# Kernel optimization log

Measured on AMD Instinct MI355X. Metric: run time of the kernel, lower is better.

The kernel has to match this reference:

```python
import jax, jax.numpy as jnp
import numpy as np

B, T, IN, RES, OUT = 32, 512, 128, 2048, 64
SPECTRAL_RADIUS = 0.9
LEAKING_RATE = 0.3
INPUT_SCALING = 1.0
WINDOW, OVERLAP = 8, 2


def setup_inputs() -> dict:
    key = jax.random.key(0)
    k1, k2 = jax.random.split(key)
    input_data = jax.random.normal(k1, (B, T, IN), dtype=jnp.float32)
    target_data = jax.random.normal(k2, (B, T, OUT), dtype=jnp.float32)
    rng = np.random.default_rng(0)
    W_res = rng.random((RES, RES), dtype=np.float32) - 0.5
    W_res *= SPECTRAL_RADIUS / np.max(np.abs(np.linalg.eigvals(W_res)))
    W_in = (rng.random((IN, RES), dtype=np.float32) - 0.5) * INPUT_SCALING
    lam_raw = jnp.zeros((), jnp.float32)
    return {"input_data": input_data, "target_data": target_data,
            "W_res": jnp.asarray(W_res.astype(np.float32)),
            "W_in": jnp.asarray(W_in.astype(np.float32)),
            "lam_raw": lam_raw}


def run_reservoir(input_data, W_res, W_in):
    b, t, d = input_data.shape
    out_size = WINDOW - 2 * OVERLAP  # 4
    pad = jnp.zeros((b, OVERLAP, d), input_data.dtype)
    x = jnp.concatenate([pad, input_data, pad], axis=1)  # [B, T+4, D]
    n_win = (t + 2 * OVERLAP - WINDOW) // out_size + 1  # T // 4
    idx = jnp.arange(n_win)[:, None] * out_size + jnp.arange(WINDOW)[None, :]
    xw = x[:, idx, :]  # [B, nW, 8, D] windows (unfold)
    state = jnp.zeros((b, n_win, W_res.shape[0]), input_data.dtype)
    states = []
    for s in range(WINDOW - OVERLAP):  # 6 sequential steps (fixed, small)
        state = (1.0 - LEAKING_RATE) * state + LEAKING_RATE * jnp.sin(
            jnp.einsum('bwr,rq->bwq', state, W_res)
            + jnp.einsum('bwd,dq->bwq', xw[:, :, s, :], W_in))
        states.append(state)
    rs = jnp.stack(states, axis=2)[:, :, OVERLAP:, :]  # keep last 4 per window
    return rs.reshape(b, t, W_res.shape[0])  # [B, T, R]


def ridge_weights(X, Y, reg_coeff):
    b, n, d = X.shape
    Xb = jnp.concatenate([X, jnp.ones((b, n, 1), X.dtype)], axis=-1)  # [B,n,d+1]
    if n >= d + 1:
        A = jnp.einsum('bnd,bne->bde', Xb, Xb) + reg_coeff * jnp.eye(d + 1, dtype=X.dtype)
        Bm = jnp.einsum('bnd,bno->bdo', Xb, Y)
        weights = jnp.linalg.solve(A, Bm)
    else:  # Woodbury: n < d+1
        A = jnp.einsum('bnd,bmd->bnm', Xb, Xb) + reg_coeff * jnp.eye(n, dtype=X.dtype)
        weights = jnp.einsum('bnd,bno->bdo', Xb, jnp.linalg.solve(A, Y))
    return weights[:, :-1], weights[:, -1:]


def reference(input_data, target_data, W_res, W_in, lam_raw):
    rs = run_reservoir(input_data, W_res, W_in)  # [B, T, R]
    reg_coeff = jax.nn.softplus(lam_raw)
    w, bias = ridge_weights(rs, target_data, reg_coeff)
    return (w, bias)
```

## Files before the change

### kernel.cpp

```cpp
#include <hip/hip_runtime.h>
#include <cmath>

#define Bb   32
#define Tt   512
#define INd  128
#define RES  2048
#define OUTd 64

#define BM 64
#define BN 64
#define BK 16

typedef unsigned short u16;
typedef __attribute__((ext_vector_type(4))) unsigned short u16x4;
typedef __attribute__((ext_vector_type(8))) unsigned short u16x8;
typedef __attribute__((ext_vector_type(8))) short bf8;
typedef __attribute__((ext_vector_type(4))) float f32x4;

__device__ __forceinline__ void splitf(float a, u16& h, u16& l) {
    unsigned u = __float_as_uint(a);
    unsigned r = (u + 0x7fffu + ((u >> 16) & 1u)) & 0xffff0000u;
    h = (u16)(r >> 16);
    float d = a - __uint_as_float(r);
    l = (u16)(__float_as_uint(d) >> 16);
}
__device__ __forceinline__ float bf2f(u16 h) {
    return __uint_as_float((unsigned)h << 16);
}
__device__ __forceinline__ void split8(const float4& a, const float4& b,
                                       u16x8& h, u16x8& l) {
    u16 hh, ll;
    splitf(a.x, hh, ll); h[0] = hh; l[0] = ll;
    splitf(a.y, hh, ll); h[1] = hh; l[1] = ll;
    splitf(a.z, hh, ll); h[2] = hh; l[2] = ll;
    splitf(a.w, hh, ll); h[3] = hh; l[3] = ll;
    splitf(b.x, hh, ll); h[4] = hh; l[4] = ll;
    splitf(b.y, hh, ll); h[5] = hh; l[5] = ll;
    splitf(b.z, hh, ll); h[6] = hh; l[6] = ll;
    splitf(b.w, hh, ll); h[7] = hh; l[7] = ll;
}

__device__ __forceinline__ void gl_lds16(const u16* g, u16* l) {
    __builtin_amdgcn_global_load_lds(
        (const __attribute__((address_space(1))) unsigned int*)g,
        (__attribute__((address_space(3))) unsigned int*)l,
        16, 0, 0);
}

#define MICRO(SA, SB)                                                           \
  do {                                                                          \
    _Pragma("unroll")                                                           \
    for (int kk = 0; kk < BK; ++kk) {                                           \
      const float4 a4 = *(const float4*)&SA[kk][ty << 2];                       \
      const float4 b4 = *(const float4*)&SB[kk][tx << 2];                       \
      acc[0][0] += a4.x*b4.x; acc[0][1] += a4.x*b4.y;                           \
      acc[0][2] += a4.x*b4.z; acc[0][3] += a4.x*b4.w;                           \
      acc[1][0] += a4.y*b4.x; acc[1][1] += a4.y*b4.y;                           \
      acc[1][2] += a4.y*b4.z; acc[1][3] += a4.y*b4.w;                           \
      acc[2][0] += a4.z*b4.x; acc[2][1] += a4.z*b4.y;                           \
      acc[2][2] += a4.z*b4.z; acc[2][3] += a4.z*b4.w;                           \
      acc[3][0] += a4.w*b4.x; acc[3][1] += a4.w*b4.y;                           \
      acc[3][2] += a4.w*b4.z; acc[3][3] += a4.w*b4.w;                           \
    }                                                                           \
  } while (0)

#define MFMA_TILE(BUF)                                                           \
  do {                                                                           \
    bf8 aH[4], aL[4], bH[4], bL[4];                                              \
    const int qd = (quad ^ ((l15 >> 1) & 3)) << 3;                               \
    _Pragma("unroll")                                                            \
    for (int i = 0; i < 4; ++i) {                                                \
      const int ar = (wm*64 + i*16 + l15)*32 + qd;                               \
      const int br = (wn*64 + i*16 + l15)*32 + qd;                               \
      aH[i] = *(const bf8*)&(BUF)[ar];                                           \
      aL[i] = *(const bf8*)&(BUF)[4096 + ar];                                    \
      bH[i] = *(const bf8*)&(BUF)[8192 + br];                                    \
      bL[i] = *(const bf8*)&(BUF)[12288 + br];                                   \
    }                                                                            \
    _Pragma("unroll")                                                            \
    for (int i = 0; i < 4; ++i)                                                  \
      _Pragma("unroll")                                                          \
      for (int j = 0; j < 4; ++j) {                                              \
        acc[i][j] = __builtin_amdgcn_mfma_f32_16x16x32_bf16(aH[i], bH[j], acc[i][j], 0, 0, 0); \
        acc[i][j] = __builtin_amdgcn_mfma_f32_16x16x32_bf16(aH[i], bL[j], acc[i][j], 0, 0, 0); \
        acc[i][j] = __builtin_amdgcn_mfma_f32_16x16x32_bf16(aL[i], bH[j], acc[i][j], 0, 0, 0); \
      }                                                                          \
  } while (0)

__global__ __launch_bounds__(256)
void tconv_kernel(const float* __restrict__ in, u16* __restrict__ outH,
                  u16* __restrict__ outL, int K, int N)
{
    __shared__ float T[64][65];
    const int n0 = blockIdx.x * 64, k0 = blockIdx.y * 64;
    const int t = threadIdx.x;
    const int r = t >> 2, c0 = (t & 3) * 16;
#pragma unroll
    for (int i = 0; i < 4; ++i) {
        const float4 v = *(const float4*)&in[(size_t)(k0 + r) * N + n0 + c0 + 4*i];
        T[r][c0 + 4*i + 0] = v.x; T[r][c0 + 4*i + 1] = v.y;
        T[r][c0 + 4*i + 2] = v.z; T[r][c0 + 4*i + 3] = v.w;
    }
    __syncthreads();
    const int n = t >> 2, ck = (t & 3) * 16;
    u16x8 h0, h1, l0, l1;
#pragma unroll
    for (int i = 0; i < 8; ++i) { u16 h, l; splitf(T[ck + i][n], h, l); h0[i] = h; l0[i] = l; }
#pragma unroll
    for (int i = 0; i < 8; ++i) { u16 h, l; splitf(T[ck + 8 + i][n], h, l); h1[i] = h; l1[i] = l; }
    const size_t ob = (size_t)(n0 + n) * K + k0 + ck;
    *(u16x8*)&outH[ob] = h0; *(u16x8*)&outH[ob + 8] = h1;
    *(u16x8*)&outL[ob] = l0; *(u16x8*)&outL[ob + 8] = l1;
}

__global__ __launch_bounds__(256)
void step_mfma_kernel(u16* __restrict__ Sh, u16* __restrict__ Sl,
                      const float* __restrict__ X,
                      const u16* __restrict__ WTh, const u16* __restrict__ WTl,
                      const u16* __restrict__ WinTh, const u16* __restrict__ WinTl,
                      int cin, int cout, int s)
{
    __shared__ u16 LB[2 * 16384];
    u16* buf0 = LB;
    u16* buf1 = LB + 16384;
    float* Cf = (float*)LB;

    const int tid = threadIdx.x;
    const int f  = (int)blockIdx.x + ((int)blockIdx.y << 4);
    const int bx = (f & 1) | (((f >> 3) & 7) << 1);
    const int by = ((f >> 1) & 3) | (((f >> 6) & 7) << 2);
    const int q0  = bx * 128;
    const int b   = by;
    const int bofs = b * Tt;
    const int wid = tid >> 6, lane = tid & 63;
    const int wm = wid & 1, wn = wid >> 1;
    const int l15 = lane & 15, quad = lane >> 4;

    f32x4 acc[4][4];
    const f32x4 zz = {0.f, 0.f, 0.f, 0.f};
#pragma unroll
    for (int i = 0; i < 4; ++i)
#pragma unroll
        for (int j = 0; j < 4; ++j) acc[i][j] = zz;

    const int rl    = lane >> 2;
    const int csrc  = (((lane & 3) ^ ((lane >> 3) & 3)) << 3);
    const u16* plane = (wid == 0) ? (const u16*)Sh
                     : (wid == 1) ? (const u16*)Sl
                     : (wid == 2) ? WTh : WTl;

    auto stage = [&](u16* buf, int k0) {
        u16* ldst = buf + wid * 4096;
#pragma unroll
        for (int i = 0; i < 8; ++i) {
            const int r = i * 16 + rl;
            const size_t grow = (wid < 2) ? (size_t)(bofs + 4 * r + cin)
                                          : (size_t)(q0 + r);
            gl_lds16(&plane[grow * RES + k0 + csrc], ldst + i * 512);
        }
    };

    if (s > 0) {
        stage(buf0, 0);
        __syncthreads();
        for (int k0 = 0; k0 < RES; k0 += 32) {
            u16* cur = (k0 & 32) ? buf1 : buf0;
            u16* nxt = (k0 & 32) ? buf0 : buf1;
            if (k0 + 32 < RES) stage(nxt, k0 + 32);
            MFMA_TILE(cur);
            __syncthreads();
        }
    }

    for (int k0 = 0; k0 < INd; k0 += 32) {
        if (tid < 128) {
            const int rrow = tid;
            const int t = 4 * rrow + s - 2;
            u16x8 h0 = {0,0,0,0,0,0,0,0}, h1 = h0, h2 = h0, h3 = h0;
            u16x8 l0 = h0, l1 = h0, l2 = h0, l3 = h0;
            if (t >= 0) {
                const float* xr = X + (size_t)(bofs + t) * INd + k0;
                const float4 f0 = *(const float4*)&xr[0];
                const float4 f1 = *(const float4*)&xr[4];
                const float4 f2 = *(const float4*)&xr[8];
                const float4 f3 = *(const float4*)&xr[12];
                const float4 f4 = *(const float4*)&xr[16];
                const float4 f5 = *(const float4*)&xr[20];
                const float4 f6 = *(const float4*)&xr[24];
                const float4 f7 = *(const float4*)&xr[28];
                split8(f0, f1, h0, l0); split8(f2, f3, h1, l1);
                split8(f4, f5, h2, l2); split8(f6, f7, h3, l3);
            }
            const int sw = (rrow >> 1) & 3;
            u16* dA = buf0 + rrow * 32;
            *(u16x8*)&dA[(0 ^ sw) << 3] = h0;
            *(u16x8*)&dA[(1 ^ sw) << 3] = h1;
            *(u16x8*)&dA[(2 ^ sw) << 3] = h2;
            *(u16x8*)&dA[(3 ^ sw) << 3] = h3;
            u16* dL = buf0 + 4096 + rrow * 32;
            *(u16x8*)&dL[(0 ^ sw) << 3] = l0;
            *(u16x8*)&dL[(1 ^ sw) << 3] = l1;
            *(u16x8*)&dL[(2 ^ sw) << 3] = l2;
            *(u16x8*)&dL[(3 ^ sw) << 3] = l3;
        } else {
            const u16* wpl = (wid == 2) ? WinTh : WinTl;
            u16* ldst = buf0 + wid * 4096;
#pragma unroll
            for (int i = 0; i < 8; ++i) {
                const int r = i * 16 + rl;
                gl_lds16(&wpl[(size_t)(q0 + r) * INd + k0 + csrc], ldst + i * 512);
            }
        }
        __syncthreads();
        MFMA_TILE(buf0);
        __syncthreads();
    }

    for (int h = 0; h < 2; ++h) {
        __syncthreads();
        if (wm == h) {
#pragma unroll
            for (int i = 0; i < 4; ++i)
#pragma unroll
                for (int j = 0; j < 4; ++j)
#pragma unroll
                    for (int rg = 0; rg < 4; ++rg)
                        Cf[(i * 16 + quad * 4 + rg) * 128 + wn * 64 + j * 16 + l15]
                            = acc[i][j][rg];
        }
        __syncthreads();
#pragma unroll
        for (int pass = 0; pass < 4; ++pass) {
            const int r  = (tid >> 4) + pass * 16;
            const int c0 = (tid & 15) * 8;
            const int wrow = h * 64 + r;
            const float4 v0 = *(const float4*)&Cf[r * 128 + c0];
            const float4 v1 = *(const float4*)&Cf[r * 128 + c0 + 4];
            float vv[8] = {v0.x, v0.y, v0.z, v0.w, v1.x, v1.y, v1.z, v1.w};
            u16x8 ph, pl;
            if (s > 0) {
                const size_t prow = (size_t)(bofs + 4 * wrow + cin) * RES + q0 + c0;
                ph = *(const u16x8*)&Sh[prow];
                pl = *(const u16x8*)&Sl[prow];
            }
            u16x8 oh, ol;
#pragma unroll
            for (int e = 0; e < 8; ++e) {
                float prev = (s > 0) ? (bf2f(ph[e]) + bf2f(pl[e])) : 0.f;
                float v = 0.7f * prev + 0.3f * sinf(vv[e]);
                u16 hh, ll; splitf(v, hh, ll);
                oh[e] = hh; ol[e] = ll;
            }
            const size_t orow = (size_t)(bofs + 4 * wrow + cout) * RES + q0 + c0;
            *(u16x8*)&Sh[orow] = oh;
            *(u16x8*)&Sl[orow] = ol;
        }
    }
}

__global__ __launch_bounds__(256)
void gram_mfma_kernel(const u16* __restrict__ Sh, const u16* __restrict__ Sl,
                      float* __restrict__ A, const float* __restrict__ lam)
{
    __shared__ u16 LB[2 * 16384];
    u16* buf0 = LB;
    u16* buf1 = LB + 16384;
    float* Cf = (float*)LB;

    const int tid = threadIdx.x;
    const int bt  = blockIdx.y;
    int ti = 0, rem = (int)blockIdx.x;
    while (rem >= 4 - ti) { rem -= 4 - ti; ++ti; }
    const int tj = ti + rem;
    const int n0 = ti * 128, m0 = tj * 128;
    const int bofs = bt * Tt;

    const int wid = tid >> 6, lane = tid & 63;
    const int wm = wid & 1, wn = wid >> 1;
    const int l15 = lane & 15, quad = lane >> 4;

    f32x4 acc[4][4];
    const f32x4 zz = {0.f, 0.f, 0.f, 0.f};
#pragma unroll
    for (int i = 0; i < 4; ++i)
#pragma unroll
        for (int j = 0; j < 4; ++j) acc[i][j] = zz;

    const int rl    = lane >> 2;
    const int csrc  = (((lane & 3) ^ ((lane >> 3) & 3)) << 3);
    const u16* plane = (wid & 1) ? Sl : Sh;
    const int rbase  = (wid < 2) ? n0 : m0;

    auto stage = [&](u16* buf, int k0) {
        u16* ldst = buf + wid * 4096;
#pragma unroll
        for (int i = 0; i < 8; ++i) {
            const int r = i * 16 + rl;
            gl_lds16(&plane[(size_t)(bofs + rbase + r) * RES + k0 + csrc],
                     ldst + i * 512);
        }
    };

    stage(buf0, 0);
    __syncthreads();
    for (int k0 = 0; k0 < RES; k0 += 32) {
        u16* cur = (k0 & 32) ? buf1 : buf0;
        u16* nxt = (k0 & 32) ? buf0 : buf1;
        if (k0 + 32 < RES) stage(nxt, k0 + 32);
        MFMA_TILE(cur);
        __syncthreads();
    }

    const float reg = log1pf(expf(lam[0]));
    float* Ab = A + (size_t)bt * 512 * 512;
    for (int h = 0; h < 2; ++h) {
        __syncthreads();
        if (wm == h) {
#pragma unroll
            for (int i = 0; i < 4; ++i)
#pragma unroll
                for (int j = 0; j < 4; ++j)
#pragma unroll
                    for (int rg = 0; rg < 4; ++rg)
                        Cf[(i * 16 + quad * 4 + rg) * 132 + wn * 64 + j * 16 + l15]
                            = acc[i][j][rg];
        }
        __syncthreads();
#pragma unroll
        for (int pass = 0; pass < 4; ++pass) {
            const int r  = (tid >> 4) + pass * 16;
            const int c0 = (tid & 15) * 8;
            const int nn = n0 + h * 64 + r;
            float o[8];
#pragma unroll
            for (int e = 0; e < 8; ++e) {
                const int mm = m0 + c0 + e;
                float v = Cf[r * 132 + c0 + e] + 1.0f;
                if (nn == mm) v += reg;
                o[e] = v;
            }
            float* dst = Ab + (size_t)nn * 512 + m0 + c0;
            *(float4*)&dst[0] = make_float4(o[0], o[1], o[2], o[3]);
            *(float4*)&dst[4] = make_float4(o[4], o[5], o[6], o[7]);
        }
#pragma unroll
        for (int pass = 0; pass < 4; ++pass) {
            const int rt  = (tid >> 3) + pass * 32;
            const int c0t = (tid & 7) * 8;
            const int mm  = m0 + rt;
            float o[8];
#pragma unroll
            for (int e = 0; e < 8; ++e) {
                const int nn = n0 + h * 64 + c0t + e;
                float v = Cf[(c0t + e) * 132 + rt] + 1.0f;
                if (nn == mm) v += reg;
                o[e] = v;
            }
            float* dst = Ab + (size_t)mm * 512 + n0 + h * 64 + c0t;
            *(float4*)&dst[0] = make_float4(o[0], o[1], o[2], o[3]);
            *(float4*)&dst[4] = make_float4(o[4], o[5], o[6], o[7]);
        }
    }
}

__global__ __launch_bounds__(256)
void chol_diag_inv_kernel(float* __restrict__ Aall, float* __restrict__ Winv,
                          float* __restrict__ WinvT, int k)
{
    __shared__ float P[64][65];
    __shared__ float W[64][65];
    const int b = blockIdx.x, tid = threadIdx.x;
    float* A = Aall + (size_t)b * 512 * 512;
    const int j0 = 64 * k;
    const int r = tid & 63;
    const int q = tid >> 6;

    {
        const int lr = tid >> 2, lc = (tid & 3) * 16;
#pragma unroll
        for (int i = 0; i < 4; ++i) {
            const float4 v = *(const float4*)(A + (size_t)(j0 + lr) * 512 + j0 + lc + 4*i);
            P[lr][lc + 4*i + 0] = v.x; P[lr][lc + 4*i + 1] = v.y;
            P[lr][lc + 4*i + 2] = v.z; P[lr][lc + 4*i + 3] = v.w;
        }
    }
    __syncthreads();

    for (int j = 0; j < 64; ++j) {
        if (tid < 64) {
            const float d = sqrtf(P[j][j]);
            if (tid == j)      P[j][j]   = d;
            else if (tid > j)  P[tid][j] = P[tid][j] / d;
        }
        __syncthreads();
        const float prj = P[r][j];
        float pm[16];
#pragma unroll
        for (int i = 0; i < 16; ++i) pm[i] = P[q * 16 + i][j];
#pragma unroll
        for (int i = 0; i < 16; ++i) {
            const int m = q * 16 + i;
            if (m > j && m <= r) P[r][m] -= prj * pm[i];
        }
        __syncthreads();
    }

    for (int t = tid; t < 4096; t += 256)
        W[t >> 6][t & 63] = ((t >> 6) == (t & 63)) ? 1.f : 0.f;
    __syncthreads();
    for (int j = 0; j < 64; ++j) {
        if (tid < 64) W[j][tid] = W[j][tid] / P[j][j];
        __syncthreads();
        const float wjc = W[j][r];
        float pm[16];
#pragma unroll
        for (int i = 0; i < 16; ++i) pm[i] = P[q * 16 + i][j];
#pragma unroll
        for (int i = 0; i < 16; ++i) {
            const int m = q * 16 + i;
            if (m > j) W[m][r] -= pm[i] * wjc;
        }
        __syncthreads();
    }

    {
        const int lr = tid >> 2, lc = (tid & 3) * 16;
#pragma unroll
        for (int i = 0; i < 4; ++i)
            *(float4*)(A + (size_t)(j0 + lr) * 512 + j0 + lc + 4*i) =
                make_float4(P[lr][lc + 4*i + 0], P[lr][lc + 4*i + 1],
                            P[lr][lc + 4*i + 2], P[lr][lc + 4*i + 3]);
    }
    float* Wo  = Winv  + ((size_t)b * 8 + k) * 64 * 64;
    float* WoT = WinvT + ((size_t)b * 8 + k) * 64 * 64;
    for (int t = tid; t < 4096; t += 256) {
        Wo[t]  = W[t >> 6][t & 63];
        WoT[t] = W[t & 63][t >> 6];
    }
}

__global__ __launch_bounds__(256)
void trsm_kernel(float* __restrict__ Aall, const float* __restrict__ WinvT, int k)
{
    __shared__ float St[BK][BM + 4];
    __shared__ float Wt[BK][BN + 4];
    float* A = Aall + (size_t)blockIdx.y * 512 * 512;
    const float* WT = WinvT + ((size_t)blockIdx.y * 8 + k) * 64 * 64;
    const int i0 = (k + 1 + blockIdx.x) * 64, p0 = k * 64;
    const int tid = threadIdx.x;
    const int li = tid >> 2, lk = (tid & 3) << 2;
    const int wk = tid >> 4, wq = (tid & 15) << 2;
    const int ty = tid >> 4, tx = tid & 15;
    float acc[4][4] = {};
    for (int k0 = 0; k0 < 64; k0 += BK) {
        const float4 u = *(const float4*)(A + (size_t)(i0 + li) * 512 + p0 + k0 + lk);
        St[lk + 0][li] = u.x; St[lk + 1][li] = u.y;
        St[lk + 2][li] = u.z; St[lk + 3][li] = u.w;
        *(float4*)&Wt[wk][wq] = *(const float4*)(WT + (size_t)(k0 + wk) * 64 + wq);
        __syncthreads();
        MICRO(St, Wt);
        __syncthreads();
    }
#pragma unroll
    for (int a = 0; a < 4; ++a) {
        const int r = i0 + (ty << 2) + a;
        *(float4*)(A + (size_t)r * 512 + p0 + (tx << 2)) =
            make_float4(acc[a][0], acc[a][1], acc[a][2], acc[a][3]);
    }
}

__global__ __launch_bounds__(256)
void chol_trailing_kernel(float* __restrict__ Aall, int k)
{
    __shared__ float Ut[BK][BM + 4];
    __shared__ float Vt[BK][BN + 4];
    float* A = Aall + (size_t)blockIdx.y * 512 * 512;
    const int tid = threadIdx.x;
    int a = 0, rem = (int)blockIdx.x;
    while (rem >= a + 1) { rem -= a + 1; ++a; }
    const int ti = k + 1 + a, tj = k + 1 + rem;
    const int i0 = ti * 64, j0c = tj * 64, p0 = k * 64;

    const int li = tid >> 2, lk = (tid & 3) << 2;
    const int ty = tid >> 4, tx = tid & 15;
    float acc[4][4] = {};

    for (int k0 = 0; k0 < 64; k0 += BK) {
        const float4 u = *(const float4*)(A + (size_t)(i0 + li) * 512 + p0 + k0 + lk);
        const float4 v = *(const float4*)(A + (size_t)(j0c + li) * 512 + p0 + k0 + lk);
        Ut[lk + 0][li] = u.x; Ut[lk + 1][li] = u.y;
        Ut[lk + 2][li] = u.z; Ut[lk + 3][li] = u.w;
        Vt[lk + 0][li] = v.x; Vt[lk + 1][li] = v.y;
        Vt[lk + 2][li] = v.z; Vt[lk + 3][li] = v.w;
        __syncthreads();
        MICRO(Ut, Vt);
        __syncthreads();
    }
#pragma unroll
    for (int aa = 0; aa < 4; ++aa) {
        const int r = i0 + (ty << 2) + aa;
        float* crow = A + (size_t)r * 512 + j0c + (tx << 2);
        float4 cv = *(const float4*)crow;
        cv.x -= acc[aa][0]; cv.y -= acc[aa][1];
        cv.z -= acc[aa][2]; cv.w -= acc[aa][3];
        *(float4*)crow = cv;
    }
}

__global__ __launch_bounds__(256, 1)
void fb_solve4_kernel(const float* __restrict__ Aall,
                      const float* __restrict__ Winv,
                      const float* __restrict__ WinvT,
                      const float* __restrict__ Y, float* __restrict__ Zall)
{
    __shared__ float V[512][10];
    __shared__ float U[64][10];
    const int tid = threadIdx.x;
    const int b   = (int)blockIdx.x & 31;
    const int c0  = ((int)blockIdx.x >> 5) * 8;
    const int ty  = tid >> 2;
    const int tx  = tid & 3;
    const float* A   = Aall + (size_t)b * 512 * 512;
    const float* Yb  = Y    + (size_t)b * 512 * OUTd + c0;
    float*       Zb  = Zall + (size_t)b * 512 * OUTd + c0;
    const float* Wb  = Winv  + (size_t)b * 8 * 4096 + (size_t)ty * 64;
    const float* WbT = WinvT + (size_t)b * 8 * 4096 + (size_t)ty * 64;

    for (int t = tid; t < 512 * 4; t += 256) {
        const int row = t >> 2, p = (t & 3) * 2;
        *(float2*)&V[row][p] = *(const float2*)&Yb[(size_t)row * OUTd + p];
    }
    __syncthreads();

    float acc0, acc1;
    f32x4 p0[4], p1[4], p2[4], p3[4];

#define LDF(P, c, G)                                                            \
    { const int cc_ = ((c) < (G)) ? (c) : (G) - 1;                              \
      _Pragma("unroll") for (int j_ = 0; j_ < 4; ++j_)                          \
        P[j_] = *(const f32x4*)&Arow[16 * cc_ + 4 * j_]; }

#define LDB(P, c, G)                                                            \
    { const int cc_ = ((c) < (G)) ? (c) : (G) - 1;                              \
      _Pragma("unroll") for (int j_ = 0; j_ < 16; ++j_)                         \
        P[j_ >> 2][j_ & 3] = Acol[(size_t)(m1 + 16 * cc_ + j_) * 512]; }

#define CMPV(P, kb)                                                             \
    { _Pragma("unroll") for (int q_ = 0; q_ < 16; ++q_) {                       \
        const float a_ = P[q_ >> 2][q_ & 3];                                    \
        const float2 v_ = *(const float2*)&V[(kb) + q_][2 * tx];                \
        acc0 += a_ * v_.x; acc1 += a_ * v_.y; } }

#define CMPU(P, kb)                                                             \
    { _Pragma("unroll") for (int q_ = 0; q_ < 16; ++q_) {                       \
        const float a_ = P[q_ >> 2][q_ & 3];                                    \
        const float2 v_ = *(const float2*)&U[(kb) + q_][2 * tx];                \
        acc0 += a_ * v_.x; acc1 += a_ * v_.y; } }

#define DIAG(Wrow)                                                              \
    { acc0 = 0.f; acc1 = 0.f;                                                   \
      _Pragma("unroll") for (int j_ = 0; j_ < 4; ++j_) {                        \
        p0[j_] = *(const f32x4*)&(Wrow)[ 0 + 4 * j_];                           \
        p1[j_] = *(const f32x4*)&(Wrow)[16 + 4 * j_];                           \
        p2[j_] = *(const f32x4*)&(Wrow)[32 + 4 * j_];                           \
        p3[j_] = *(const f32x4*)&(Wrow)[48 + 4 * j_]; }                         \
      CMPU(p0, 0); CMPU(p1, 16); CMPU(p2, 32); CMPU(p3, 48); }

    for (int k = 0; k < 8; ++k) {
        const int r0 = k * 64;
        const float* Arow = A + (size_t)(r0 + ty) * 512;
        acc0 = 0.f; acc1 = 0.f;
        const int G = r0 >> 4;
        if (G) {
            LDF(p0, 0, G); LDF(p1, 1, G); LDF(p2, 2, G); LDF(p3, 3, G);
            for (int g = 0; g < G; g += 4) {
                CMPV(p0, 16 * g);      LDF(p0, g + 4, G);
                CMPV(p1, 16 * g + 16); LDF(p1, g + 5, G);
                CMPV(p2, 16 * g + 32); LDF(p2, g + 6, G);
                CMPV(p3, 16 * g + 48); LDF(p3, g + 7, G);
            }
        }
        U[ty][2 * tx]     = V[r0 + ty][2 * tx]     - acc0;
        U[ty][2 * tx + 1] = V[r0 + ty][2 * tx + 1] - acc1;
        __syncthreads();
        DIAG(Wb + (size_t)k * 4096);
        V[r0 + ty][2 * tx]     = acc0;
        V[r0 + ty][2 * tx + 1] = acc1;
        __syncthreads();
    }

    for (int k = 7; k >= 0; --k) {
        const int r0 = k * 64;
        const float* Acol = A + r0 + ty;
        const int m1 = r0 + 64;
        acc0 = 0.f; acc1 = 0.f;
        const int G = (448 - r0) >> 4;
        if (G) {
            LDB(p0, 0, G); LDB(p1, 1, G); LDB(p2, 2, G); LDB(p3, 3, G);
            for (int g = 0; g < G; g += 4) {
                CMPV(p0, m1 + 16 * g);      LDB(p0, g + 4, G);
                CMPV(p1, m1 + 16 * g + 16); LDB(p1, g + 5, G);
                CMPV(p2, m1 + 16 * g + 32); LDB(p2, g + 6, G);
                CMPV(p3, m1 + 16 * g + 48); LDB(p3, g + 7, G);
            }
        }
        U[ty][2 * tx]     = V[r0 + ty][2 * tx]     - acc0;
        U[ty][2 * tx + 1] = V[r0 + ty][2 * tx + 1] - acc1;
        __syncthreads();
        DIAG(WbT + (size_t)k * 4096);
        V[r0 + ty][2 * tx]     = acc0;
        V[r0 + ty][2 * tx + 1] = acc1;
        __syncthreads();
    }

    for (int t = tid; t < 512 * 4; t += 256) {
        const int row = t >> 2, p = (t & 3) * 2;
        *(float2*)&Zb[(size_t)row * OUTd + p] = *(const float2*)&V[row][p];
    }
#undef LDF
#undef LDB
#undef CMPV
#undef CMPU
#undef DIAG
}

__global__ __launch_bounds__(256)
void out_kernel(const u16* __restrict__ Sh, const u16* __restrict__ Sl,
                const float* __restrict__ Z, float* __restrict__ Wout)
{
    __shared__ float Rt[BK][64 + 4];
    __shared__ float Zt[BK][64 + 4];
    const int tid = threadIdx.x;
    const int b   = blockIdx.y;
    const int d0  = blockIdx.x * 64;
    const int kk  = tid >> 4, cq = (tid & 15) << 2;
    const int ty  = tid >> 4, tx = tid & 15;
    float acc[4][4] = {};

    for (int k0 = 0; k0 < Tt; k0 += BK) {
        const size_t ri = (size_t)(b * Tt + k0 + kk) * RES + d0 + cq;
        const u16x4 hv = *(const u16x4*)&Sh[ri];
        const u16x4 lv = *(const u16x4*)&Sl[ri];
        Rt[kk][cq + 0] = bf2f(hv[0]) + bf2f(lv[0]);
        Rt[kk][cq + 1] = bf2f(hv[1]) + bf2f(lv[1]);
        Rt[kk][cq + 2] = bf2f(hv[2]) + bf2f(lv[2]);
        Rt[kk][cq + 3] = bf2f(hv[3]) + bf2f(lv[3]);
        *(float4*)&Zt[kk][cq] =
            *(const float4*)(Z + ((size_t)b * Tt + k0 + kk) * OUTd + cq);
        __syncthreads();
        MICRO(Rt, Zt);
        __syncthreads();
    }
#pragma unroll
    for (int a = 0; a < 4; ++a) {
        const int d = d0 + (ty << 2) + a;
        *(float4*)(Wout + ((size_t)b * RES + d) * OUTd + (tx << 2)) =
            make_float4(acc[a][0], acc[a][1], acc[a][2], acc[a][3]);
    }
}

__global__ __launch_bounds__(256)
void bias_kernel(const float* __restrict__ Z, float* __restrict__ Bout)
{
    __shared__ float S[4][64];
    const int b = blockIdx.x;
    const int o = threadIdx.x & 63, g = threadIdx.x >> 6;
    const float* Zb = Z + (size_t)b * Tt * OUTd;
    float s = 0.f;
    for (int n = g * 128; n < (g + 1) * 128; ++n) s += Zb[(size_t)n * OUTd + o];
    S[g][o] = s;
    __syncthreads();
    if (threadIdx.x < 64)
        Bout[(size_t)b * OUTd + o] = ((S[0][o] + S[1][o]) + S[2][o]) + S[3][o];
}

extern "C" void kernel_launch(void* const* d_in, const int* in_sizes, int n_in,
                              void* d_out, int out_size, void* d_ws, size_t ws_size,
                              hipStream_t stream)
{
    const float* X    = (const float*)d_in[0];
    const float* Y    = (const float*)d_in[1];
    const float* Wres = (const float*)d_in[2];
    const float* Win  = (const float*)d_in[3];
    const float* lam  = (const float*)d_in[4];

    float* out  = (float*)d_out;
    float* Wout = out;
    float* Bout = out + (size_t)Bb * RES * OUTd;

    char* p = (char*)d_ws;
    u16* Sh    = (u16*)p;   p += (size_t)Bb * Tt * RES * 2;
    u16* Sl    = (u16*)p;   p += (size_t)Bb * Tt * RES * 2;
    u16* WTh   = (u16*)p;   p += (size_t)RES * RES * 2;
    u16* WTl   = (u16*)p;   p += (size_t)RES * RES * 2;
    u16* WinTh = (u16*)p;   p += (size_t)INd * RES * 2;
    u16* WinTl = (u16*)p;   p += (size_t)INd * RES * 2;
    float* A   = (float*)p; p += (size_t)Bb * 512 * 512 * 4;
    float* Z   = (float*)p; p += (size_t)Bb * Tt * OUTd * 4;
    float* Wi  = (float*)p; p += (size_t)Bb * 8 * 64 * 64 * 4;
    float* WiT = (float*)p;

    const dim3 blk(256);
    tconv_kernel<<<dim3(RES / 64, RES / 64), blk, 0, stream>>>(Wres, WTh, WTl, RES, RES);
    tconv_kernel<<<dim3(RES / 64, INd / 64), blk, 0, stream>>>(Win, WinTh, WinTl, INd, RES);

    const dim3 sgrid(RES / 128, Bb);
    step_mfma_kernel<<<sgrid, blk, 0, stream>>>(Sh, Sl, X, WTh, WTl, WinTh, WinTl, 0, 2, 0);
    step_mfma_kernel<<<sgrid, blk, 0, stream>>>(Sh, Sl, X, WTh, WTl, WinTh, WinTl, 2, 1, 1);
    step_mfma_kernel<<<sgrid, blk, 0, stream>>>(Sh, Sl, X, WTh, WTl, WinTh, WinTl, 1, 0, 2);
    step_mfma_kernel<<<sgrid, blk, 0, stream>>>(Sh, Sl, X, WTh, WTl, WinTh, WinTl, 0, 1, 3);
    step_mfma_kernel<<<sgrid, blk, 0, stream>>>(Sh, Sl, X, WTh, WTl, WinTh, WinTl, 1, 2, 4);
    step_mfma_kernel<<<sgrid, blk, 0, stream>>>(Sh, Sl, X, WTh, WTl, WinTh, WinTl, 2, 3, 5);

    gram_mfma_kernel<<<dim3(10, Bb), blk, 0, stream>>>(Sh, Sl, A, lam);

    for (int k = 0; k < 8; ++k) {
        chol_diag_inv_kernel<<<dim3(Bb), dim3(256), 0, stream>>>(A, Wi, WiT, k);
        if (k < 7) {
            trsm_kernel<<<dim3(7 - k, Bb), blk, 0, stream>>>(A, WiT, k);
            const int m = 7 - k;
            chol_trailing_kernel<<<dim3(m * (m + 1) / 2, Bb), blk, 0, stream>>>(A, k);
        }
    }
    fb_solve4_kernel<<<dim3(Bb * 8), dim3(256), 0, stream>>>(A, Wi, WiT, Y, Z);

    out_kernel<<<dim3(RES / 64, Bb), blk, 0, stream>>>(Sh, Sl, Z, Wout);
    bias_kernel<<<dim3(Bb), dim3(256), 0, stream>>>(Z, Bout);
}
```

Before: 2.044 ms.

## Fuse Cholesky and triangular inverse into one sqrt-free LDL-style loop

The diagonal-block kernel used to run the Cholesky factorization and the inversion of its triangular factor as two separate 64-step loops, each step with two barriers. It now runs a single fused loop with one barrier per step, doing an unnormalized (LDL-like) elimination on P and W at the same time. Square roots and scaling by the diagonal are deferred to the write-out. This cuts barriers and serial steps in the small per-block factorization, at the cost of extra divides and sqrts in the store phase. Numerical behaviour changes slightly.

Measured after the change: 1.929 ms. 1.06x faster.

```diff
diff --git a/kernel.cpp b/kernel.cpp
--- a/kernel.cpp
+++ b/kernel.cpp
@@ -384,41 +384,26 @@
             P[lr][lc + 4*i + 2] = v.z; P[lr][lc + 4*i + 3] = v.w;
         }
     }
-    __syncthreads();
-
-    for (int j = 0; j < 64; ++j) {
-        if (tid < 64) {
-            const float d = sqrtf(P[j][j]);
-            if (tid == j)      P[j][j]   = d;
-            else if (tid > j)  P[tid][j] = P[tid][j] / d;
-        }
-        __syncthreads();
-        const float prj = P[r][j];
-        float pm[16];
-#pragma unroll
-        for (int i = 0; i < 16; ++i) pm[i] = P[q * 16 + i][j];
-#pragma unroll
-        for (int i = 0; i < 16; ++i) {
-            const int m = q * 16 + i;
-            if (m > j && m <= r) P[r][m] -= prj * pm[i];
-        }
-        __syncthreads();
-    }
-
     for (int t = tid; t < 4096; t += 256)
         W[t >> 6][t & 63] = ((t >> 6) == (t & 63)) ? 1.f : 0.f;
     __syncthreads();
+
     for (int j = 0; j < 64; ++j) {
-        if (tid < 64) W[j][tid] = W[j][tid] / P[j][j];
-        __syncthreads();
-        const float wjc = W[j][r];
+        const float rd2 = 1.0f / P[j][j];
+        const float tfa = P[r][j] * rd2;
+        const float cwd = W[j][r] * rd2;
         float pm[16];
 #pragma unroll
         for (int i = 0; i < 16; ++i) pm[i] = P[q * 16 + i][j];
 #pragma unroll
         for (int i = 0; i < 16; ++i) {
             const int m = q * 16 + i;
-            if (m > j) W[m][r] -= pm[i] * wjc;
+            if (m > j && m <= r) P[r][m] -= tfa * pm[i];
+        }
+#pragma unroll
+        for (int i = 0; i < 16; ++i) {
+            const int m = q * 16 + i;
+            if (m > j) W[m][r] -= pm[i] * cwd;
         }
         __syncthreads();
     }
@@ -426,16 +411,26 @@
     {
         const int lr = tid >> 2, lc = (tid & 3) * 16;
 #pragma unroll
-        for (int i = 0; i < 4; ++i)
+        for (int i = 0; i < 4; ++i) {
+            float o[4];
+#pragma unroll
+            for (int e = 0; e < 4; ++e) {
+                const int c = lc + 4*i + e;
+                const float pv = P[lr][c];
+                if (c < lr)       o[e] = pv / sqrtf(P[c][c]);
+                else if (c == lr) o[e] = sqrtf(pv);
+                else              o[e] = pv;
+            }
             *(float4*)(A + (size_t)(j0 + lr) * 512 + j0 + lc + 4*i) =
-                make_float4(P[lr][lc + 4*i + 0], P[lr][lc + 4*i + 1],
-                            P[lr][lc + 4*i + 2], P[lr][lc + 4*i + 3]);
+                make_float4(o[0], o[1], o[2], o[3]);
+        }
     }
     float* Wo  = Winv  + ((size_t)b * 8 + k) * 64 * 64;
     float* WoT = WinvT + ((size_t)b * 8 + k) * 64 * 64;
     for (int t = tid; t < 4096; t += 256) {
-        Wo[t]  = W[t >> 6][t & 63];
-        WoT[t] = W[t & 63][t >> 6];
+        const int rr = t >> 6, cc = t & 63;
+        Wo[t]  = W[rr][cc] / sqrtf(P[rr][rr]);
+        WoT[t] = W[cc][rr] / sqrtf(P[cc][cc]);
     }
 }
 
```
